# Optimization experiments

Hardware: AMD Instinct MI355X
Metric: run time of the kernel (lower is better)

Reference implementation:

```python
import jax, jax.numpy as jnp
import numpy as np

BS, PV, NPTS, C = 8, 40000, 32, 4   # batch, pillars/sample (=max_voxels), max_num_points, point channels
X_L, Y_L = 432, 496                  # BEV grid from voxel_size / point_cloud_range


def setup_inputs() -> dict:
    key = jax.random.key(0)
    k1, k2, k3 = jax.random.split(key, 3)
    # (P, num_points, c) voxelized point features
    pillars = jax.random.normal(k1, (BS * PV, NPTS, C), dtype=jnp.float32)
    # unique BEV cell per pillar within each sample (voxelizer never emits duplicate coords)
    perms = jax.vmap(lambda k: jax.random.permutation(k, X_L * Y_L)[:PV])(
        jax.random.split(k2, BS))  # (BS, PV) linear cell ids
    xs = (perms // Y_L).reshape(-1)
    ys = (perms % Y_L).reshape(-1)
    b = jnp.repeat(jnp.arange(BS, dtype=jnp.int32), PV)
    z = jnp.zeros_like(b)
    coors_batch = jnp.stack([b, xs.astype(jnp.int32), ys.astype(jnp.int32), z], axis=1)  # (P, 4)
    npoints_per_pillar = jax.random.randint(k3, (BS * PV,), 1, NPTS + 1, dtype=jnp.int32)
    return {
        "pillars": pillars,
        "coors_batch": coors_batch,
        "npoints_per_pillar": npoints_per_pillar,
        "bs": BS, "x_l": X_L, "y_l": Y_L,
    }


def reference(pillars, coors_batch, npoints_per_pillar, bs, x_l, y_l):
    # per-pillar xyz center of mass: sum over (zero-padded) points / true point count
    center_pt = jnp.sum(pillars[:, :, :3], axis=1) / npoints_per_pillar[:, None].astype(jnp.float32)  # (P, 3)
    # scatter centers into dense BEV canvas (bs, x_l, y_l, 3); coords unique -> set semantics match torch assignment
    canvas = jnp.zeros((bs, x_l, y_l, 3), dtype=jnp.float32)
    canvas = canvas.at[coors_batch[:, 0], coors_batch[:, 1], coors_batch[:, 2]].set(center_pt)
    # per-sample permute(2,1,0): (x_l,y_l,3) -> (3,y_l,x_l)
    batched_pillar_center = jnp.transpose(canvas, (0, 3, 2, 1))
    return (pillars, coors_batch, npoints_per_pillar, batched_pillar_center)
```

## Files before the change

kernel.cpp:

```cpp
#include <hip/hip_runtime.h>


typedef float vfloat4 __attribute__((ext_vector_type(4)));

__global__ __launch_bounds__(256) void canvas_zero(float4* __restrict__ dst, long n4) {
    long i = (long)blockIdx.x * blockDim.x + threadIdx.x;
    const long stride = (long)gridDim.x * blockDim.x;
    const float4 z = make_float4(0.f, 0.f, 0.f, 0.f);
    for (; i < n4; i += stride) dst[i] = z;
}

__global__ __launch_bounds__(256) void pillar_fused(
    const vfloat4* __restrict__ pillars4,
    const int4* __restrict__ coors4,
    const int* __restrict__ npoints,
    const int* __restrict__ xlp,
    const int* __restrict__ ylp,
    vfloat4* __restrict__ out_pillars4,
    float4* __restrict__ out_coors4,
    float* __restrict__ out_np,
    float* __restrict__ canvas,
    int P)
{
    const int group = blockIdx.x * (blockDim.x >> 5) + (threadIdx.x >> 5);
    const int lane  = threadIdx.x & 31;
    if (group >= P) return;
    const int p = group;

    const vfloat4 v = __builtin_nontemporal_load(&pillars4[p * 32 + lane]);
    __builtin_nontemporal_store(v, &out_pillars4[p * 32 + lane]);

    float sx = v.x, sy = v.y, sz = v.z;
    #pragma unroll
    for (int m = 16; m >= 1; m >>= 1) {
        sx += __shfl_xor(sx, m);
        sy += __shfl_xor(sy, m);
        sz += __shfl_xor(sz, m);
    }

    if (lane < 3) {
        const int4 c  = coors4[p];
        const int npts = npoints[p];
        const float s = (lane == 0) ? sx : (lane == 1) ? sy : sz;
        const float val = s / (float)npts;

        const int x_l = *xlp;
        const int y_l = *ylp;
        const long cs   = (long)y_l * (long)x_l;
        const long base = (long)c.x * 3l * cs + (long)c.z * (long)x_l + (long)c.y;
        canvas[base + (long)lane * cs] = val;

        if (lane == 0) {
            out_coors4[p] = make_float4((float)c.x, (float)c.y, (float)c.z, (float)c.w);
            out_np[p] = (float)npts;
        }
    }
}

extern "C" void kernel_launch(void* const* d_in, const int* in_sizes, int n_in,
                              void* d_out, int out_size, void* d_ws, size_t ws_size,
                              hipStream_t stream) {
    const vfloat4* pillars4 = (const vfloat4*)d_in[0];
    const int4* coors4      = (const int4*)d_in[1];
    const int* npoints      = (const int*)d_in[2];
    const int* xlp = (const int*)d_in[4];
    const int* ylp = (const int*)d_in[5];

    const int n_pillars = in_sizes[0];
    const int n_coors   = in_sizes[1];
    const int P         = in_sizes[2];

    float* out            = (float*)d_out;
    vfloat4* out_pillars4 = (vfloat4*)out;
    float* out_coors      = out + n_pillars;
    float* out_np         = out_coors + n_coors;
    float* canvas         = out_np + P;
    const long canvas_elems = (long)out_size - n_pillars - n_coors - P;

    const long n4 = canvas_elems >> 2;
    canvas_zero<<<(int)((n4 + 255) / 256), 256, 0, stream>>>((float4*)canvas, n4);

    const int groups_per_block = 256 / 32;
    const int blocks = (P + groups_per_block - 1) / groups_per_block;
    pillar_fused<<<blocks, 256, 0, stream>>>(
        pillars4, coors4, npoints, xlp, ylp,
        out_pillars4, (float4*)out_coors, out_np, canvas, P);
}
```

Baseline: 76.66 us.

## Process each pillar with four threads and eight loads each for ILP

The pillar kernel now assigns 4 threads per pillar instead of 32, and each thread issues 8 independent float4 loads before reducing them. This raises memory-level parallelism per thread and cuts shuffle steps from five to two. The coordinate and point-count writes move to the fourth thread so they no longer share a thread with a canvas write. The canvas zeroing launch is also capped at 2048 blocks, which switches it to a grid-stride loop. Each thread now holds more registers, and the load stride of 4 float4s per thread may coalesce less cleanly.

After: 84.44 us. 10.1% more time.

```diff
diff --git a/kernel.cpp b/kernel.cpp
--- a/kernel.cpp
+++ b/kernel.cpp
@@ -10,7 +10,7 @@
     for (; i < n4; i += stride) dst[i] = z;
 }
 
-__global__ __launch_bounds__(256) void pillar_fused(
+__global__ __launch_bounds__(256) void pillar_fused_ilp(
     const vfloat4* __restrict__ pillars4,
     const int4* __restrict__ coors4,
     const int* __restrict__ npoints,
@@ -22,38 +22,45 @@
     float* __restrict__ canvas,
     int P)
 {
-    const int group = blockIdx.x * (blockDim.x >> 5) + (threadIdx.x >> 5);
-    const int lane  = threadIdx.x & 31;
-    if (group >= P) return;
-    const int p = group;
+    constexpr int K = 8;
+    const int g = blockIdx.x * 64 + (threadIdx.x >> 2);
+    const int r = threadIdx.x & 3;
+    if (g >= P) return;
 
-    const vfloat4 v = __builtin_nontemporal_load(&pillars4[p * 32 + lane]);
-    __builtin_nontemporal_store(v, &out_pillars4[p * 32 + lane]);
+    const long base = (long)g * 32 + r;
 
-    float sx = v.x, sy = v.y, sz = v.z;
+    vfloat4 v[K];
     #pragma unroll
-    for (int m = 16; m >= 1; m >>= 1) {
+    for (int k = 0; k < K; ++k)
+        v[k] = __builtin_nontemporal_load(&pillars4[base + 4 * k]);
+
+    float sx = 0.f, sy = 0.f, sz = 0.f;
+    #pragma unroll
+    for (int k = 0; k < K; ++k) {
+        __builtin_nontemporal_store(v[k], &out_pillars4[base + 4 * k]);
+        sx += v[k].x; sy += v[k].y; sz += v[k].z;
+    }
+
+    #pragma unroll
+    for (int m = 1; m <= 2; m <<= 1) {
         sx += __shfl_xor(sx, m);
         sy += __shfl_xor(sy, m);
         sz += __shfl_xor(sz, m);
     }
 
-    if (lane < 3) {
-        const int4 c  = coors4[p];
-        const int npts = npoints[p];
-        const float s = (lane == 0) ? sx : (lane == 1) ? sy : sz;
-        const float val = s / (float)npts;
+    const int4 c   = coors4[g];
+    const int npts = npoints[g];
 
+    if (r == 3) {
+        out_coors4[g] = make_float4((float)c.x, (float)c.y, (float)c.z, (float)c.w);
+        out_np[g]     = (float)npts;
+    } else {
+        const float s   = (r == 0) ? sx : (r == 1) ? sy : sz;
         const int x_l = *xlp;
         const int y_l = *ylp;
         const long cs   = (long)y_l * (long)x_l;
-        const long base = (long)c.x * 3l * cs + (long)c.z * (long)x_l + (long)c.y;
-        canvas[base + (long)lane * cs] = val;
-
-        if (lane == 0) {
-            out_coors4[p] = make_float4((float)c.x, (float)c.y, (float)c.z, (float)c.w);
-            out_np[p] = (float)npts;
-        }
+        const long base_c = (long)c.x * 3l * cs + (long)c.z * (long)x_l + (long)c.y;
+        canvas[base_c + (long)r * cs] = s / (float)npts;
     }
 }
 
@@ -78,11 +85,13 @@
     const long canvas_elems = (long)out_size - n_pillars - n_coors - P;
 
     const long n4 = canvas_elems >> 2;
-    canvas_zero<<<(int)((n4 + 255) / 256), 256, 0, stream>>>((float4*)canvas, n4);
+    const long zthreads = (n4 + 1) / 2;
+    int zblocks = (int)((zthreads + 255) / 256);
+    if (zblocks > 2048) zblocks = 2048;
+    canvas_zero<<<zblocks, 256, 0, stream>>>((float4*)canvas, n4);
 
-    const int groups_per_block = 256 / 32;
-    const int blocks = (P + groups_per_block - 1) / groups_per_block;
-    pillar_fused<<<blocks, 256, 0, stream>>>(
+    const int blocks = (P + 63) / 64;
+    pillar_fused_ilp<<<blocks, 256, 0, stream>>>(
         pillars4, coors4, npoints, xlp, ylp,
         out_pillars4, (float4*)out_coors, out_np, canvas, P);
 }
```
